# Optimization experiments

Measured on AMD Instinct MI355X. Metric: run time of the kernel, lower is better.

Reference implementation:

```python
import jax, jax.numpy as jnp
import numpy as np

V = 32000; DM = 512; DS = 64; K = 4; INNER = 2048; KK = 3
B = 4; N = 512; LOOPS = 6; H_CYCLES = 2; POWER = 2


def _ln(x, g, b, eps=1e-5):
    mu = jnp.mean(x, -1, keepdims=True)
    var = jnp.mean(jnp.square(x - mu), -1, keepdims=True)
    return (x - mu) * jax.lax.rsqrt(var + eps) * g + b


def _sn(W, u):
    # torch spectral_norm: one power iteration (no grad through u,v), sigma differentiable through W
    v = W.T @ u
    v = v / (jnp.linalg.norm(v) + 1e-12)
    u2 = W @ v
    u2 = u2 / (jnp.linalg.norm(u2) + 1e-12)
    u2 = jax.lax.stop_gradient(u2)
    v = jax.lax.stop_gradient(v)
    sigma = u2 @ (W @ v)
    return W / sigma


def _block(Q_in, p):
    Qn = _ln(Q_in, p['g1'], p['b1'])                       # [B,N,d]
    qp = Qn.mean(1)                                        # [B,d]
    Wq = _sn(p['hqW'], p['uq'])
    Wk = _sn(p['hkW'], p['uk'])
    Oq = (qp @ Wq.T).reshape(-1, DM, DS)                   # [B,d,D]
    Ok = (qp @ Wk.T).reshape(-1, DM, DS)
    Pq = jax.nn.elu(jnp.einsum('bnd,bde->bne', Qn, Oq) + p['BQ']) + 1.0
    Pk = jax.nn.elu(jnp.einsum('bnd,bde->bne', Qn, Ok) + p['BK']) + 1.0
    Wm = jnp.maximum(jnp.einsum('bne,bme->bnm', Pq, Pk), 0.0) ** POWER  # [B,N,N]
    Att = jnp.einsum('bnm,bmd->bnd', Wm, Qn)
    Nrm = jnp.abs(Wm.sum(-1)) + 1.0                        # [B,N]
    m = Att / Nrm[..., None] - Qn
    mp = m @ p['mW'].T + p['mb']
    Qi = Q_in + jax.nn.softplus(p['dt']) * mp
    Qn2 = _ln(Qi, p['g2'], p['b2'])
    GU = Qn2 @ p['WupW'].T                                 # [B,N,2*inner]
    G, U = GU[..., :INNER], GU[..., INNER:]
    H = jax.nn.silu(G) * U
    Ht = jnp.transpose(H, (0, 2, 1))                       # [B,inner,N]
    Hc = jax.lax.conv_general_dilated(Ht, p['convW'], (1,), [(1, 1)],
                                      dimension_numbers=('NCH', 'OIH', 'NCH'),
                                      feature_group_count=INNER)
    Hc = jnp.transpose(Hc, (0, 2, 1))
    return Qi + Hc @ p['WdownW'].T


def _run(Q, bp):
    for i in range(K):
        Q = _block(Q, {k: v[i] for k, v in bp.items()})
    return Q


def setup_inputs() -> dict:
    key = jax.random.key(0)
    ks = iter(jax.random.split(key, 48))
    nrm = lambda s, std=0.02: jax.random.normal(next(ks), s, jnp.float32) * std
    inp = {}
    inp['inputs'] = jax.random.randint(next(ks), (B, N), 0, V, jnp.int32)
    inp['labels'] = jax.random.randint(next(ks), (B, N), 0, V, jnp.int32)
    inp['halted'] = jnp.ones((B,), bool)
    inp['steps'] = jnp.zeros((B,), jnp.int32)
    inp['carry_hidden'] = jnp.zeros((B, N, DM), jnp.float32)
    inp['carry_inputs'] = jnp.zeros((B, N), jnp.int32)
    inp['carry_labels'] = jnp.zeros((B, N), jnp.int32)
    inp['embedding'] = nrm((V, DM))
    inp['pos_emb'] = nrm((8192, DM))
    inp['in_g'] = jnp.ones((DM,), jnp.float32)
    inp['in_b'] = jnp.zeros((DM,), jnp.float32)
    inp['init_hidden'] = nrm((DM,))
    inp['dt'] = jnp.full((K,), 0.1, jnp.float32)
    inp['mW'] = nrm((K, DM, DM))
    inp['mb'] = jnp.zeros((K, DM), jnp.float32)
    inp['hqW'] = nrm((K, DM * DS, DM))
    inp['hkW'] = nrm((K, DM * DS, DM))
    uq = jax.random.normal(next(ks), (K, DM * DS), jnp.float32)
    uk = jax.random.normal(next(ks), (K, DM * DS), jnp.float32)
    inp['uq'] = uq / jnp.linalg.norm(uq, axis=-1, keepdims=True)
    inp['uk'] = uk / jnp.linalg.norm(uk, axis=-1, keepdims=True)
    inp['BQ'] = nrm((K, DS))
    inp['BK'] = nrm((K, DS))
    inp['g1'] = jnp.ones((K, DM), jnp.float32)
    inp['b1'] = jnp.zeros((K, DM), jnp.float32)
    inp['g2'] = jnp.ones((K, DM), jnp.float32)
    inp['b2'] = jnp.zeros((K, DM), jnp.float32)
    inp['WupW'] = nrm((K, 2 * INNER, DM))
    inp['convW'] = nrm((K, INNER, 1, KK))
    inp['WdownW'] = nrm((K, DM, INNER))
    inp['fin_g'] = jnp.ones((DM,), jnp.float32)
    inp['fin_b'] = jnp.zeros((DM,), jnp.float32)
    inp['halt_W'] = nrm((1, DM))
    inp['halt_b'] = jnp.full((1,), -5.0, jnp.float32)
    inp['lm_head'] = nrm((V, DM))
    return inp


def reference(inputs, labels, halted, steps, carry_hidden, carry_inputs, carry_labels,
              embedding, pos_emb, in_g, in_b, init_hidden, dt, mW, mb, hqW, hkW, uq, uk,
              BQ, BK, g1, b1, g2, b2, WupW, convW, WdownW, fin_g, fin_b, halt_W, halt_b, lm_head):
    bp = dict(dt=dt, mW=mW, mb=mb, hqW=hqW, hkW=hkW, uq=uq, uk=uk, BQ=BQ, BK=BK,
              g1=g1, b1=b1, g2=g2, b2=b2, WupW=WupW, convW=convW, WdownW=WdownW)
    new_hidden = jnp.where(halted[:, None, None], init_hidden, carry_hidden)
    new_steps = jnp.where(halted, jnp.zeros_like(steps), steps)
    new_inputs = jnp.where(halted[:, None], inputs, carry_inputs)
    X = _ln(embedding[new_inputs] + pos_emb[:inputs.shape[1]][None], in_g, in_b)
    Q = new_hidden
    for _ in range(H_CYCLES - 1):  # no_grad burn-in
        Q = jax.lax.stop_gradient(_run(Q + X, bp))
    Q = _run(Q + X, bp)            # gradient pass (L_cycles = 1)
    Qf = _ln(Q, fin_g, fin_b)
    logits = Qf @ lm_head.T
    halt_logits = Qf.mean(1) @ halt_W.T + halt_b
    new_steps = new_steps + 1
    new_halted = new_steps >= LOOPS
    return logits, halt_logits, jax.lax.stop_gradient(Q), new_steps, new_halted
```

## Files before the change

kernel.cpp:

```cpp
#include <hip/hip_runtime.h>
#include <stdint.h>

#define DMD 512
#define NSEQ 512
#define NBATCH 4
#define WROWS 32768
#define VOCAB 32000

#define OFF_HALT   65536000L
#define OFF_Q      65536004L
#define OFF_STEPS  66584580L
#define OFF_HALTED 66584584L

typedef __attribute__((ext_vector_type(8))) short short8v;
typedef __attribute__((ext_vector_type(4))) float f32x4;

__device__ __forceinline__ ushort f2bf(float f){
  uint u = __builtin_bit_cast(uint, f);
  u += 0x7fffu + ((u >> 16) & 1u);
  return (ushort)(u >> 16);
}
__device__ __forceinline__ float bf2f(ushort h){
  return __builtin_bit_cast(float, (uint)h << 16);
}

__device__ __forceinline__ float block_reduce_sum256(float v, float* red){
  int t = threadIdx.x;
  red[t] = v; __syncthreads();
  for (int o = 128; o; o >>= 1){
    if (t < o) red[t] += red[t+o];
    __syncthreads();
  }
  float r = red[0]; __syncthreads();
  return r;
}

__global__ void k_ln(const float* __restrict__ in, float* __restrict__ outf,
                     ushort* __restrict__ outb,
                     const float* __restrict__ g, const float* __restrict__ b){
  __shared__ float red[256];
  long r = blockIdx.x; int t = threadIdx.x;
  const float* x = in + r*DMD;
  float v0 = x[t], v1 = x[t+256];
  float mu = block_reduce_sum256(v0+v1, red) * (1.f/DMD);
  float d0 = v0-mu, d1 = v1-mu;
  float var = block_reduce_sum256(d0*d0+d1*d1, red) * (1.f/DMD);
  float rs = rsqrtf(var + 1e-5f);
  float o0 = d0*rs*g[t] + b[t];
  float o1 = d1*rs*g[t+256] + b[t+256];
  if (outf){ outf[r*DMD+t] = o0; outf[r*DMD+t+256] = o1; }
  if (outb){ outb[r*DMD+t] = f2bf(o0); outb[r*DMD+t+256] = f2bf(o1); }
}

__global__ void k_ln_add(float* __restrict__ Qa, const float* __restrict__ X,
                         float* __restrict__ outf, ushort* __restrict__ outb,
                         const float* __restrict__ g, const float* __restrict__ b){
  __shared__ float red[256];
  long r = blockIdx.x; int t = threadIdx.x;
  float* x = Qa + r*DMD;
  const float* xx = X + r*DMD;
  float v0 = x[t]+xx[t], v1 = x[t+256]+xx[t+256];
  x[t] = v0; x[t+256] = v1;
  float mu = block_reduce_sum256(v0+v1, red) * (1.f/DMD);
  float d0 = v0-mu, d1 = v1-mu;
  float var = block_reduce_sum256(d0*d0+d1*d1, red) * (1.f/DMD);
  float rs = rsqrtf(var + 1e-5f);
  float o0 = d0*rs*g[t] + b[t];
  float o1 = d1*rs*g[t+256] + b[t+256];
  if (outf){ outf[r*DMD+t] = o0; outf[r*DMD+t+256] = o1; }
  if (outb){ outb[r*DMD+t] = f2bf(o0); outb[r*DMD+t+256] = f2bf(o1); }
}

__global__ void k_embed_ln(const int* __restrict__ inputs, const int* __restrict__ cinputs,
                           const int* __restrict__ halted32,
                           const float* __restrict__ emb, const float* __restrict__ pos,
                           const float* __restrict__ g, const float* __restrict__ b,
                           float* __restrict__ X){
  __shared__ float red[256];
  int r = blockIdx.x; int t = threadIdx.x;
  int n = r & 511;
  bool hall = (halted32[0] != 0);
  int tok = hall ? inputs[r] : cinputs[r];
  const float* e = emb + (long)tok*DMD;
  const float* p = pos + (long)n*DMD;
  float v0 = e[t]+p[t], v1 = e[t+256]+p[t+256];
  float mu = block_reduce_sum256(v0+v1, red) * (1.f/DMD);
  float d0 = v0-mu, d1 = v1-mu;
  float var = block_reduce_sum256(d0*d0+d1*d1, red) * (1.f/DMD);
  float rs = rsqrtf(var + 1e-5f);
  X[(long)r*DMD+t]     = d0*rs*g[t]     + b[t];
  X[(long)r*DMD+t+256] = d1*rs*g[t+256] + b[t+256];
}

__global__ void k_sn_v(const float* __restrict__ hqW, const float* __restrict__ hkW,
                       const float* __restrict__ uq, const float* __restrict__ uk,
                       float* __restrict__ vraw, ushort* __restrict__ Wbf){
  __shared__ float red[2048];
  int z = blockIdx.y; int k = z >> 1, qk = z & 1;
  const float* W = (qk ? hkW : hqW) + (long)k*WROWS*DMD;
  const float* u = (qk ? uk : uq) + (long)k*WROWS;
  ushort* Wb = Wbf ? (Wbf + (long)z*WROWS*DMD) : nullptr;
  int t = threadIdx.x;
  int c4 = (t & 127) * 4;
  int rsub = t >> 7;
  int r0 = blockIdx.x * 256;
  float4 acc = {0.f,0.f,0.f,0.f};
  if (Wb){
    for (int r = rsub; r < 256; r += 4){
      long off = (long)(r0+r)*DMD + c4;
      float4 w = *(const float4*)(W + off);
      float uu = u[r0+r];
      acc.x += w.x*uu; acc.y += w.y*uu; acc.z += w.z*uu; acc.w += w.w*uu;
      ushort4 o; o.x = f2bf(w.x); o.y = f2bf(w.y); o.z = f2bf(w.z); o.w = f2bf(w.w);
      *(ushort4*)(Wb + off) = o;
    }
  } else {
    for (int r = rsub; r < 256; r += 4){
      long off = (long)(r0+r)*DMD + c4;
      float4 w = *(const float4*)(W + off);
      float uu = u[r0+r];
      acc.x += w.x*uu; acc.y += w.y*uu; acc.z += w.z*uu; acc.w += w.w*uu;
    }
  }
  red[rsub*512 + c4+0] = acc.x; red[rsub*512 + c4+1] = acc.y;
  red[rsub*512 + c4+2] = acc.z; red[rsub*512 + c4+3] = acc.w;
  __syncthreads();
  if (rsub == 0){
    #pragma unroll
    for (int i = 0; i < 4; i++){
      int c = c4 + i;
      float s = red[c] + red[512+c] + red[1024+c] + red[1536+c];
      atomicAdd(&vraw[z*DMD + c], s);
    }
  }
}

__global__ void k_sn_norm(float* __restrict__ vraw){
  __shared__ float red[512];
  int z = blockIdx.x; int t = threadIdx.x;
  float* v = vraw + z*DMD;
  float x = v[t];
  red[t] = x*x; __syncthreads();
  for (int o = 256; o; o >>= 1){
    if (t < o) red[t] += red[t+o];
    __syncthreads();
  }
  float nrm = sqrtf(red[0]);
  v[t] = x / (nrm + 1e-12f);
}

__global__ void k_sn_s(const float* __restrict__ hqW, const float* __restrict__ hkW,
                       const float* __restrict__ vraw, float* __restrict__ ssq){
  int z = blockIdx.y; int k = z >> 1, qk = z & 1;
  const float* W = (qk ? hkW : hqW) + (long)k*WROWS*DMD;
  const float* v = vraw + z*DMD;
  int wave = threadIdx.x >> 6, lane = threadIdx.x & 63;
  float vreg[8];
  #pragma unroll
  for (int i = 0; i < 8; i++) vreg[i] = v[lane + 64*i];
  int r0 = blockIdx.x*256 + wave*64;
  float acc = 0.f;
  for (int r = r0; r < r0+64; r++){
    float p = 0.f;
    #pragma unroll
    for (int i = 0; i < 8; i++)
      p += W[(long)r*DMD + lane + 64*i] * vreg[i];
    for (int off = 32; off; off >>= 1) p += __shfl_down(p, off);
    if (lane == 0) acc += p*p;
  }
  if (lane == 0) atomicAdd(&ssq[z], acc);
}

__global__ void k_sn_s_bf(const ushort* __restrict__ Wbf, const float* __restrict__ vraw,
                          float* __restrict__ ssq){
  int z = blockIdx.y;
  const ushort* W = Wbf + (long)z*WROWS*DMD;
  const float* v = vraw + z*DMD;
  int wave = threadIdx.x >> 6, lane = threadIdx.x & 63;
  float vreg[8];
  #pragma unroll
  for (int i = 0; i < 8; i++) vreg[i] = v[lane*8 + i];
  int r0 = blockIdx.x*256 + wave*64;
  float acc = 0.f;
  for (int r = r0; r < r0+64; r++){
    short8v wv = *(const short8v*)&W[(long)r*DMD + lane*8];
    float p = 0.f;
    #pragma unroll
    for (int i = 0; i < 8; i++)
      p += bf2f((ushort)wv[i]) * vreg[i];
    for (int off = 32; off; off >>= 1) p += __shfl_down(p, off);
    if (lane == 0) acc += p*p;
  }
  if (lane == 0) atomicAdd(&ssq[z], acc);
}

__global__ void k_sn_fin(const float* __restrict__ ssq, float* __restrict__ sgm){
  int t = threadIdx.x;
  if (t < 8){
    float s2 = ssq[t];
    sgm[t] = s2 / (sqrtf(s2) + 1e-12f);
  }
}

__global__ void k_proj(const float* __restrict__ hqW, const float* __restrict__ hkW,
                       const float* __restrict__ qp, const float* __restrict__ sgm,
                       ushort* __restrict__ OqT, ushort* __restrict__ OkT, int k){
  int z = blockIdx.y;
  const float* W = (z ? hkW : hqW) + (long)k*WROWS*DMD;
  ushort* O = z ? OkT : OqT;
  float inv = 1.f / sgm[k*2 + z];
  int wave = threadIdx.x >> 6, lane = threadIdx.x & 63;
  long r = (long)blockIdx.x*4 + wave;
  float a0=0,a1=0,a2=0,a3=0;
  for (int j = lane; j < DMD; j += 64){
    float w = W[r*DMD + j];
    a0 += w*qp[j]; a1 += w*qp[DMD+j]; a2 += w*qp[2*DMD+j]; a3 += w*qp[3*DMD+j];
  }
  for (int off = 32; off; off >>= 1){
    a0 += __shfl_down(a0,off); a1 += __shfl_down(a1,off);
    a2 += __shfl_down(a2,off); a3 += __shfl_down(a3,off);
  }
  if (lane == 0){
    int d = (int)(r >> 6), e = (int)(r & 63);
    long o = (long)e*512 + d;
    O[o] = f2bf(a0*inv); O[32768+o] = f2bf(a1*inv);
    O[2*32768+o] = f2bf(a2*inv); O[3*32768+o] = f2bf(a3*inv);
  }
}

__global__ void k_proj_bf(const ushort* __restrict__ Wbf, const float* __restrict__ qp,
                          const float* __restrict__ sgm,
                          ushort* __restrict__ OqT, ushort* __restrict__ OkT, int k){
  int z = blockIdx.y;
  const ushort* W = Wbf + (long)(k*2 + z)*WROWS*DMD;
  ushort* O = z ? OkT : OqT;
  float inv = 1.f / sgm[k*2 + z];
  int wave = threadIdx.x >> 6, lane = threadIdx.x & 63;
  float qpr[4][8];
  #pragma unroll
  for (int b = 0; b < 4; b++)
    #pragma unroll
    for (int i = 0; i < 8; i++)
      qpr[b][i] = qp[b*512 + lane*8 + i];
  long r = (long)blockIdx.x*4 + wave;
  short8v wv = *(const short8v*)&W[r*DMD + lane*8];
  float w[8];
  #pragma unroll
  for (int i = 0; i < 8; i++) w[i] = bf2f((ushort)wv[i]);
  float a0=0,a1=0,a2=0,a3=0;
  #pragma unroll
  for (int i = 0; i < 8; i++){
    a0 += w[i]*qpr[0][i]; a1 += w[i]*qpr[1][i];
    a2 += w[i]*qpr[2][i]; a3 += w[i]*qpr[3][i];
  }
  for (int off = 32; off; off >>= 1){
    a0 += __shfl_down(a0,off); a1 += __shfl_down(a1,off);
    a2 += __shfl_down(a2,off); a3 += __shfl_down(a3,off);
  }
  if (lane == 0){
    int d = (int)(r >> 6), e = (int)(r & 63);
    long o = (long)e*512 + d;
    O[o] = f2bf(a0*inv); O[32768+o] = f2bf(a1*inv);
    O[2*32768+o] = f2bf(a2*inv); O[3*32768+o] = f2bf(a3*inv);
  }
}

template<int BM, int BN, int WM, int WN, int EPI, int BFOUT, int DUAL>
__global__ __launch_bounds__(256) void mm_bt(
    const ushort* __restrict__ A, const ushort* __restrict__ B, void* __restrict__ C,
    int N, int K, long sA, long sB, long sC,
    const float* __restrict__ bias, const float* __restrict__ bias2,
    const float* __restrict__ res, const float* __restrict__ dtp, int dtidx,
    float* __restrict__ aux)
{
  __shared__ ushort As[BM*64];
  __shared__ ushort Bs[BN*64];
  const int z = blockIdx.z;
  const float* biasz = bias;
  if (DUAL){
    A += (long)(z & 3)*sA;
    if (z >= 4) biasz = bias2;
  } else {
    A += (long)z*sA;
  }
  B += (long)z*sB;
  const int tm = blockIdx.y*BM, tn = DUAL ? 0 : blockIdx.x*BN;
  const int tid = threadIdx.x;
  const int wid = tid >> 6, lane = tid & 63;
// ... 37 lines not shown
      }
      #pragma unroll
      for (int j = 0; j < FN; j++){
        int row = wc*WN + j*16 + ln15;
        bfr[j] = *(const short8v*)&Bs[row*64 + (((ks*4+kq) ^ (row&7))*8)];
      }
      #pragma unroll
      for (int i = 0; i < FM; i++)
        #pragma unroll
        for (int j = 0; j < FN; j++)
          acc[i][j] = __builtin_amdgcn_mfma_f32_16x16x32_bf16(af[i], bfr[j], acc[i][j], 0, 0, 0);
    }
    __syncthreads();
  }

  float sp = 0.f;
  if (EPI == 3) sp = log1pf(expf(dtp[dtidx]));
  float* Cf = (float*)C + (long)z*sC;
  ushort* Cb = (ushort*)C + (long)z*sC;
  const float* rz = res ? (res + (long)z*sC) : nullptr;
  const float* nrmz = (EPI == 5) ? (bias + (long)z*512) : nullptr;
  #pragma unroll
  for (int i = 0; i < FM; i++){
    int row0 = tm + wr*WM + i*16 + kq*4;
    #pragma unroll
    for (int j = 0; j < FN; j++){
      int col = tn + wc*WN + j*16 + ln15;
      #pragma unroll
      for (int r = 0; r < 4; r++){
        int row = row0 + r;
        long idx = (long)row*N + col;
        float v = acc[i][j][r];
        if (EPI == 1){ v += biasz[col]; v = v > 0.f ? v : expm1f(v); v += 1.f; }
        else if (EPI == 2){ v = fmaxf(v, 0.f); v = v*v; }
        else if (EPI == 3){ v = rz[idx] + sp*(v + biasz[col]); }
        else if (EPI == 4){ v = v + rz[idx]; if (aux) aux[idx] = v; }
        else if (EPI == 5){ v = v / nrmz[row] - rz[idx]; }
        if (BFOUT) Cb[idx] = f2bf(v);
        else       Cf[idx] = v;
      }
    }
  }
}

__global__ void k_tr(const float* __restrict__ Qn, ushort* __restrict__ QnT){
  __shared__ float t[64][65];
  int b = blockIdx.z;
  int n0 = blockIdx.x*64, d0 = blockIdx.y*64;
  int tx = threadIdx.x & 63, ty = threadIdx.x >> 6;
  #pragma unroll
  for (int i = 0; i < 64; i += 4)
    t[ty+i][tx] = Qn[(long)b*262144 + (long)(n0+ty+i)*512 + d0+tx];
  __syncthreads();
  #pragma unroll
  for (int i = 0; i < 64; i += 4)
    QnT[(long)b*262144 + (long)(d0+ty+i)*512 + n0+tx] = f2bf(t[tx][ty+i]);
}

__global__ void k_qinit(const int* __restrict__ halted32, const float* __restrict__ ih,
                        const float* __restrict__ ch, float* __restrict__ Qa){
  long i = (long)blockIdx.x*512 + threadIdx.x;
  int c = (int)(i & 511);
  Qa[i] = (halted32[0] != 0) ? ih[c] : ch[i];
}

__global__ void k_qp1(const float* __restrict__ Qn, float* __restrict__ part){
  int b = blockIdx.x, c = blockIdx.y, t = threadIdx.x;
  const float* base = Qn + (long)b*262144 + (long)c*32*512;
  float acc = 0.f;
  #pragma unroll
  for (int n = 0; n < 32; n++) acc += base[n*512 + t];
  part[((long)b*16 + c)*512 + t] = acc;
}
__global__ void k_qp2(const float* __restrict__ part, float* __restrict__ qp){
  int b = blockIdx.x, t = threadIdx.x;
  float s = 0.f;
  #pragma unroll
  for (int c = 0; c < 16; c++) s += part[((long)b*16 + c)*512 + t];
  qp[b*512 + t] = s * (1.f/512.f);
}

__global__ void k_rowsum_bf(const ushort* __restrict__ Wm, float* __restrict__ Nrm){
  __shared__ float red[256];
  long r = blockIdx.x; int t = threadIdx.x;
  const ushort* x = Wm + r*NSEQ;
  float s = block_reduce_sum256(bf2f(x[t]) + bf2f(x[t+256]), red);
  if (t == 0) Nrm[r] = fabsf(s) + 1.f;
}

__global__ void k_convfuse(const ushort* __restrict__ GU, const float* __restrict__ w,
                           ushort* __restrict__ Hc){
  int r = blockIdx.x;
  int n = r & 511;
  int c = threadIdx.x * 8;
  long base = (long)r*4096 + c;
  float o[8] = {};
  {
    if (n > 0){
      short8v gv = *(const short8v*)&GU[base-4096];
      short8v uv = *(const short8v*)&GU[base-4096+2048];
      #pragma unroll
      for (int i = 0; i < 8; i++){
        float g = bf2f((ushort)gv[i]), u = bf2f((ushort)uv[i]);
        o[i] += g/(1.f+expf(-g))*u * w[(c+i)*3+0];
      }
    }
    {
      short8v gv = *(const short8v*)&GU[base];
      short8v uv = *(const short8v*)&GU[base+2048];
      #pragma unroll
      for (int i = 0; i < 8; i++){
        float g = bf2f((ushort)gv[i]), u = bf2f((ushort)uv[i]);
        o[i] += g/(1.f+expf(-g))*u * w[(c+i)*3+1];
      }
    }
    if (n < 511){
      short8v gv = *(const short8v*)&GU[base+4096];
      short8v uv = *(const short8v*)&GU[base+4096+2048];
      #pragma unroll
      for (int i = 0; i < 8; i++){
        float g = bf2f((ushort)gv[i]), u = bf2f((ushort)uv[i]);
        o[i] += g/(1.f+expf(-g))*u * w[(c+i)*3+2];
      }
    }
  }
  short8v ov;
  #pragma unroll
  for (int i = 0; i < 8; i++) ov[i] = (short)f2bf(o[i]);
  *(short8v*)&Hc[(long)r*2048 + c] = ov;
}

__global__ void k_cvt(const float* __restrict__ in, ushort* __restrict__ out){
  long i = ((long)blockIdx.x*256 + threadIdx.x)*4;
  float4 v = *(const float4*)(in + i);
  ushort4 o;
  o.x = f2bf(v.x); o.y = f2bf(v.y); o.z = f2bf(v.z); o.w = f2bf(v.w);
  *(ushort4*)(out + i) = o;
}

__global__ void k_halt1(const float* __restrict__ Qf, const float* __restrict__ hW,
                        float* __restrict__ hpart){
  __shared__ float red[256];
  int b = blockIdx.x, c = blockIdx.y, t = threadIdx.x;
  const float* base = Qf + (long)b*262144 + (long)c*32*512;
  float acc = 0.f;
  for (int i = t; i < 32*512; i += 256)
    acc += base[i] * hW[i & 511];
  float s = block_reduce_sum256(acc, red);
  if (t == 0) hpart[b*16 + c] = s;
}

__global__ void k_fin(const int* __restrict__ halted32, const int* __restrict__ steps,
                      const float* __restrict__ hpart, const float* __restrict__ hb,
                      float* __restrict__ o_halt, float* __restrict__ o_steps,
                      float* __restrict__ o_halted){
  int t = threadIdx.x;
  if (t < NBATCH){
    float s = 0.f;
    for (int c = 0; c < 16; c++) s += hpart[t*16 + c];
    o_halt[t] = s*(1.f/512.f) + hb[0];
    bool hall = (halted32[0] != 0);
    int ns = (hall ? 0 : steps[t]) + 1;
    o_steps[t] = (float)ns;
    o_halted[t] = ns >= 6 ? 1.f : 0.f;
  }
}

extern "C" void kernel_launch(void* const* d_in, const int* in_sizes, int n_in,
                              void* d_out, int out_size, void* d_ws, size_t ws_size,
                              hipStream_t stream)
{
  const int*     inputs       = (const int*)d_in[0];
  const int*     halted32     = (const int*)d_in[2];
  const int*     steps        = (const int*)d_in[3];
  const float*   carry_hidden = (const float*)d_in[4];
// ... 18 lines not shown
  const float*   b2   = (const float*)d_in[24];
  const float*   WupW = (const float*)d_in[25];
  const float*   convW= (const float*)d_in[26];
  const float*   WdownW=(const float*)d_in[27];
  const float*   fin_g= (const float*)d_in[28];
  const float*   fin_b= (const float*)d_in[29];
  const float*   halt_W=(const float*)d_in[30];
  const float*   halt_b=(const float*)d_in[31];
  const float*   lm_head=(const float*)d_in[32];
  float* out = (float*)d_out;

  float* ws = (float*)d_ws;
  float*  X    = ws;
  float*  Qa   = ws +  1048576;
  float*  Qb   = ws +  2097152;
  float*  Qn   = ws +  3145728;
  ushort* GU_bf  = (ushort*)(ws +  4194304);
  ushort* Hc_bf  = (ushort*)(ws +  8388608);
  ushort* m_bf   = (ushort*)(ws + 10485760);
  ushort* Wm_bf  = (ushort*)(ws + 11010048);
  ushort* QnT_bf = (ushort*)(ws + 11534336);
  ushort* Pq_bf  = (ushort*)(ws + 12058624);
  ushort* OqT    = (ushort*)(ws + 12189696);
  ushort* lm_bf  = (ushort*)(ws +  4194304);
  ushort* Qn_bf  = (ushort*)(ws + 13369344);
  ushort* mW_bf  = (ushort*)(ws + 13893632);
  ushort* Wup_bf = (ushort*)(ws + 14417920);
  ushort* Wdn_bf = (ushort*)(ws + 18612224);
  float*  qp   = ws + 20709376;
  float*  Nrm  = ws + 20711424;
  float*  vraw = ws + 20713472;
  float*  ssq  = ws + 20717568;
  float*  sgm  = ws + 20717632;
  float*  qp_part = ws + 20717696;
  float*  hpart   = ws + 20750464;
  ushort* W_bf = (ushort*)(ws + 20750528);
  const size_t NEED_BF = (size_t)(20750528 + 67108864) * 4;
  const bool useBf = ws_size >= NEED_BF;

  k_cvt<<<1024, 256, 0, stream>>>(mW, mW_bf);
  k_cvt<<<8192, 256, 0, stream>>>(WupW, Wup_bf);
  k_cvt<<<4096, 256, 0, stream>>>(WdownW, Wdn_bf);

  hipMemsetAsync(vraw, 0, (4096+64)*sizeof(float), stream);
  k_sn_v<<<dim3(128,8), 512, 0, stream>>>(hqW, hkW, uq, uk, vraw,
                                          useBf ? W_bf : nullptr);
  k_sn_norm<<<8, 512, 0, stream>>>(vraw);
  if (useBf)
    k_sn_s_bf<<<dim3(128,8), 256, 0, stream>>>(W_bf, vraw, ssq);
  else
    k_sn_s<<<dim3(128,8), 256, 0, stream>>>(hqW, hkW, vraw, ssq);
  k_sn_fin<<<1, 64, 0, stream>>>(ssq, sgm);

  k_embed_ln<<<2048, 256, 0, stream>>>(inputs, carry_inputs, halted32,
                                       embedding, pos_emb, in_g, in_b, X);
  k_qinit<<<2048, 512, 0, stream>>>(halted32, init_hidden, carry_hidden, Qa);

  for (int cyc = 0; cyc < 2; cyc++){
    for (int k = 0; k < 4; k++){
      if (k == 0)
        k_ln_add<<<2048, 256, 0, stream>>>(Qa, X, Qn, Qn_bf, g1 + k*DMD, b1 + k*DMD);
      else
        k_ln<<<2048, 256, 0, stream>>>(Qa, Qn, Qn_bf, g1 + k*DMD, b1 + k*DMD);
      k_tr<<<dim3(8,8,4), 256, 0, stream>>>(Qn, QnT_bf);
      k_qp1<<<dim3(4,16), 512, 0, stream>>>(Qn, qp_part);
      k_qp2<<<4, 512, 0, stream>>>(qp_part, qp);
      if (useBf)
        k_proj_bf<<<dim3(8192,2), 256, 0, stream>>>(W_bf, qp, sgm, OqT, OqT + 131072, k);
      else
        k_proj<<<dim3(8192,2), 256, 0, stream>>>(hqW, hkW, qp, sgm, OqT, OqT + 131072, k);
      mm_bt<64,64,32,32,1,1,1><<<dim3(1,8,8), 256, 0, stream>>>(
          Qn_bf, OqT, Pq_bf, 64, 512, 262144, 32768, 32768,
          BQb + k*64, BKb + k*64, nullptr, nullptr, 0, nullptr);
      mm_bt<64,64,32,32,2,1,0><<<dim3(8,8,4), 256, 0, stream>>>(
          Pq_bf, Pq_bf + 131072, Wm_bf, 512, 64, 32768, 32768, 262144,
          nullptr, nullptr, nullptr, nullptr, 0, nullptr);
      k_rowsum_bf<<<2048, 256, 0, stream>>>(Wm_bf, Nrm);
      mm_bt<64,64,32,32,5,1,0><<<dim3(8,8,4), 256, 0, stream>>>(
          Wm_bf, QnT_bf, m_bf, 512, 512, 262144, 262144, 262144,
          Nrm, nullptr, Qn, nullptr, 0, nullptr);
      mm_bt<64,64,32,32,3,0,0><<<dim3(8,32,1), 256, 0, stream>>>(
          m_bf, mW_bf + (long)k*262144, Qb, 512, 512, 0, 0, 0,
          mb + k*DMD, nullptr, Qa, dt, k, nullptr);
      k_ln<<<2048, 256, 0, stream>>>(Qb, nullptr, Qn_bf, g2 + k*DMD, b2 + k*DMD);
      mm_bt<128,128,64,64,0,1,0><<<dim3(32,16,1), 256, 0, stream>>>(
          Qn_bf, Wup_bf + (long)k*2097152, GU_bf, 4096, 512, 0, 0, 0,
          nullptr, nullptr, nullptr, nullptr, 0, nullptr);
      k_convfuse<<<2048, 256, 0, stream>>>(GU_bf, convW + (long)k*2048*3, Hc_bf);
      float* aux = (cyc == 1 && k == 3) ? (out + OFF_Q) : nullptr;
      mm_bt<64,64,32,32,4,0,0><<<dim3(8,32,1), 256, 0, stream>>>(
          Hc_bf, Wdn_bf + (long)k*1048576, Qa, 512, 2048, 0, 0, 0,
          nullptr, nullptr, Qb, nullptr, 0, aux);
    }
  }

  k_ln<<<2048, 256, 0, stream>>>(Qa, Qn, Qn_bf, fin_g, fin_b);
  k_cvt<<<16000, 256, 0, stream>>>(lm_head, lm_bf);
  mm_bt<128,128,64,64,0,0,0><<<dim3(250,16,1), 256, 0, stream>>>(
      Qn_bf, lm_bf, out, 32000, 512, 0, 0, 0,
      nullptr, nullptr, nullptr, nullptr, 0, nullptr);
  k_halt1<<<dim3(4,16), 256, 0, stream>>>(Qn, halt_W, hpart);
  k_fin<<<1, 64, 0, stream>>>(halted32, steps, hpart, halt_b,
                              out + OFF_HALT, out + OFF_STEPS, out + OFF_HALTED);
}
```

Measured before the change: 1.730 ms.

## Fuse layernorm with transpose, pooling, halt head; fold spectral norm and rowsum into GEMMs

Replaces the per-row layernorm kernels with a multi-row warp-level kernel that also writes the transposed bf16 copy, partial sequence means, the residual add and initial-state selection, and the halt dot product. This removes the separate transpose, qp1, qinit and halt kernels along with the fp32 Qn buffer. The spectral-norm sigma is now computed inside the first-cycle projection kernel and applied in the Pq/Pk GEMM epilogue, and the Wm row sums are accumulated with atomics in the Wm GEMM epilogue instead of a separate rowsum kernel. The costs are more atomics, a 64-entry sum repeated in every epilogue thread, and residuals read from bf16 Qn instead of fp32, which slightly lowers precision.

```diff
diff --git a/kernel.cpp b/kernel.cpp
--- a/kernel.cpp
+++ b/kernel.cpp
@@ -35,40 +35,99 @@
   return r;
 }
 
-__global__ void k_ln(const float* __restrict__ in, float* __restrict__ outf,
-                     ushort* __restrict__ outb,
-                     const float* __restrict__ g, const float* __restrict__ b){
-  __shared__ float red[256];
-  long r = blockIdx.x; int t = threadIdx.x;
-  const float* x = in + r*DMD;
-  float v0 = x[t], v1 = x[t+256];
-  float mu = block_reduce_sum256(v0+v1, red) * (1.f/DMD);
-  float d0 = v0-mu, d1 = v1-mu;
-  float var = block_reduce_sum256(d0*d0+d1*d1, red) * (1.f/DMD);
-  float rs = rsqrtf(var + 1e-5f);
-  float o0 = d0*rs*g[t] + b[t];
-  float o1 = d1*rs*g[t+256] + b[t+256];
-  if (outf){ outf[r*DMD+t] = o0; outf[r*DMD+t+256] = o1; }
-  if (outb){ outb[r*DMD+t] = f2bf(o0); outb[r*DMD+t+256] = f2bf(o1); }
-}
-
-__global__ void k_ln_add(float* __restrict__ Qa, const float* __restrict__ X,
-                         float* __restrict__ outf, ushort* __restrict__ outb,
-                         const float* __restrict__ g, const float* __restrict__ b){
-  __shared__ float red[256];
-  long r = blockIdx.x; int t = threadIdx.x;
-  float* x = Qa + r*DMD;
-  const float* xx = X + r*DMD;
-  float v0 = x[t]+xx[t], v1 = x[t+256]+xx[t+256];
-  x[t] = v0; x[t+256] = v1;
-  float mu = block_reduce_sum256(v0+v1, red) * (1.f/DMD);
-  float d0 = v0-mu, d1 = v1-mu;
-  float var = block_reduce_sum256(d0*d0+d1*d1, red) * (1.f/DMD);
-  float rs = rsqrtf(var + 1e-5f);
-  float o0 = d0*rs*g[t] + b[t];
-  float o1 = d1*rs*g[t+256] + b[t+256];
-  if (outf){ outf[r*DMD+t] = o0; outf[r*DMD+t+256] = o1; }
-  if (outb){ outb[r*DMD+t] = f2bf(o0); outb[r*DMD+t+256] = f2bf(o1); }
+template<int MODE, int TR, int QP, int HALT>
+__global__ __launch_bounds__(512) void k_ln1(
+    const float* in, float* QaW, const float* X,
+    const int* halted32, const float* ih, const float* ch,
+    ushort* __restrict__ outb, ushort* __restrict__ outT,
+    float* __restrict__ qp_part,
+    const float* __restrict__ g, const float* __restrict__ b,
+    const float* __restrict__ hW, float* __restrict__ hpart)
+{
+  __shared__ ushort lt[TR ? 32 : 1][TR ? 514 : 1];
+  __shared__ float red[QP ? 4096 : 1];
+  const int bb = blockIdx.y, rg = blockIdx.x;
+  const int n0 = rg*32;
+  const int tid = threadIdx.x, wave = tid >> 6, lane = tid & 63;
+  const int c8 = lane*8;
+  float qacc[8] = {};
+  #pragma unroll
+  for (int rr = 0; rr < 4; rr++){
+    const int n = n0 + wave*4 + rr;
+    const long rowo = (long)bb*262144 + (long)n*512;
+    float x[8];
+    if (MODE == 1){
+      bool hall = (halted32[0] != 0);
+      #pragma unroll
+      for (int i = 0; i < 8; i++){
+        float base = hall ? ih[c8+i] : ch[rowo + c8 + i];
+        x[i] = base + X[rowo + c8 + i];
+      }
+      #pragma unroll
+      for (int i = 0; i < 8; i++) QaW[rowo + c8 + i] = x[i];
+    } else if (MODE == 2){
+      #pragma unroll
+      for (int i = 0; i < 8; i++) x[i] = in[rowo + c8 + i] + X[rowo + c8 + i];
+      #pragma unroll
+      for (int i = 0; i < 8; i++) QaW[rowo + c8 + i] = x[i];
+    } else {
+      float4 a0 = *(const float4*)(in + rowo + c8);
+      float4 a1 = *(const float4*)(in + rowo + c8 + 4);
+      x[0]=a0.x; x[1]=a0.y; x[2]=a0.z; x[3]=a0.w;
+      x[4]=a1.x; x[5]=a1.y; x[6]=a1.z; x[7]=a1.w;
+    }
+    float s = 0.f, sq = 0.f;
+    #pragma unroll
+    for (int i = 0; i < 8; i++){ s += x[i]; sq += x[i]*x[i]; }
+    #pragma unroll
+    for (int m = 32; m; m >>= 1){
+      s  += __shfl_xor(s, m);
+      sq += __shfl_xor(sq, m);
+    }
+    float mu = s*(1.f/512.f);
+    float var = sq*(1.f/512.f) - mu*mu;
+    float rs = rsqrtf(var + 1e-5f);
+    float hd = 0.f;
+    short8v ov;
+    #pragma unroll
+    for (int i = 0; i < 8; i++){
+      float o = (x[i]-mu)*rs*g[c8+i] + b[c8+i];
+      ov[i] = (short)f2bf(o);
+      if (QP) qacc[i] += o;
+      if (HALT) hd += o * hW[c8+i];
+    }
+    *(short8v*)&outb[rowo + c8] = ov;
+    if (TR) *(short8v*)&lt[n & 31][c8] = ov;
+    if (HALT){
+      #pragma unroll
+      for (int m = 32; m; m >>= 1) hd += __shfl_xor(hd, m);
+      if (lane == 0) atomicAdd(&hpart[bb], hd);
+    }
+  }
+  if (QP){
+    #pragma unroll
+    for (int i = 0; i < 8; i++) red[wave*512 + c8 + i] = qacc[i];
+    __syncthreads();
+    if (wave == 0){
+      #pragma unroll
+      for (int i = 0; i < 8; i++){
+        int c = c8 + i;
+        float s = 0.f;
+        #pragma unroll
+        for (int w = 0; w < 8; w++) s += red[w*512 + c];
+        qp_part[((long)bb*16 + rg)*512 + c] = s;
+      }
+    }
+  }
+  if (TR){
+    __syncthreads();
+    #pragma unroll 4
+    for (int p = 0; p < 32; p++){
+      int d = p*16 + (tid >> 5);
+      int n = tid & 31;
+      outT[(long)bb*262144 + (long)d*512 + n0 + n] = lt[n][d];
+    }
+  }
 }
 
 __global__ void k_embed_ln(const int* __restrict__ inputs, const int* __restrict__ cinputs,
@@ -92,44 +151,45 @@
   X[(long)r*DMD+t+256] = d1*rs*g[t+256] + b[t+256];
 }
 
-__global__ void k_sn_v(const float* __restrict__ hqW, const float* __restrict__ hkW,
-                       const float* __restrict__ uq, const float* __restrict__ uk,
-                       float* __restrict__ vraw, ushort* __restrict__ Wbf){
-  __shared__ float red[2048];
+__global__ __launch_bounds__(512) void k_sn_v(
+    const float* __restrict__ hqW, const float* __restrict__ hkW,
+    const float* __restrict__ uq, const float* __restrict__ uk,
+    float* __restrict__ vraw, ushort* __restrict__ Wbf){
+  __shared__ float red[4096];
   int z = blockIdx.y; int k = z >> 1, qk = z & 1;
   const float* W = (qk ? hkW : hqW) + (long)k*WROWS*DMD;
   const float* u = (qk ? uk : uq) + (long)k*WROWS;
   ushort* Wb = Wbf ? (Wbf + (long)z*WROWS*DMD) : nullptr;
   int t = threadIdx.x;
-  int c4 = (t & 127) * 4;
-  int rsub = t >> 7;
+  int c8 = (t & 63) * 8;
+  int rsub = t >> 6;
   int r0 = blockIdx.x * 256;
-  float4 acc = {0.f,0.f,0.f,0.f};
-  if (Wb){
-    for (int r = rsub; r < 256; r += 4){
-      long off = (long)(r0+r)*DMD + c4;
-      float4 w = *(const float4*)(W + off);
-      float uu = u[r0+r];
-      acc.x += w.x*uu; acc.y += w.y*uu; acc.z += w.z*uu; acc.w += w.w*uu;
-      ushort4 o; o.x = f2bf(w.x); o.y = f2bf(w.y); o.z = f2bf(w.z); o.w = f2bf(w.w);
-      *(ushort4*)(Wb + off) = o;
-    }
-  } else {
-    for (int r = rsub; r < 256; r += 4){
-      long off = (long)(r0+r)*DMD + c4;
-      float4 w = *(const float4*)(W + off);
-      float uu = u[r0+r];
-      acc.x += w.x*uu; acc.y += w.y*uu; acc.z += w.z*uu; acc.w += w.w*uu;
-    }
-  }
-  red[rsub*512 + c4+0] = acc.x; red[rsub*512 + c4+1] = acc.y;
-  red[rsub*512 + c4+2] = acc.z; red[rsub*512 + c4+3] = acc.w;
+  float acc[8] = {};
+  for (int r = rsub; r < 256; r += 8){
+    long off = (long)(r0+r)*DMD + c8;
+    float4 w0 = *(const float4*)(W + off);
+    float4 w1 = *(const float4*)(W + off + 4);
+    float uu = u[r0+r];
+    float wv[8] = {w0.x,w0.y,w0.z,w0.w,w1.x,w1.y,w1.z,w1.w};
+    #pragma unroll
+    for (int i = 0; i < 8; i++) acc[i] += wv[i]*uu;
+    if (Wb){
+      short8v o;
+      #pragma unroll
+      for (int i = 0; i < 8; i++) o[i] = (short)f2bf(wv[i]);
+      *(short8v*)(Wb + off) = o;
+    }
+  }
+  #pragma unroll
+  for (int i = 0; i < 8; i++) red[rsub*512 + c8 + i] = acc[i];
   __syncthreads();
   if (rsub == 0){
     #pragma unroll
-    for (int i = 0; i < 4; i++){
-      int c = c4 + i;
-      float s = red[c] + red[512+c] + red[1024+c] + red[1536+c];
+    for (int i = 0; i < 8; i++){
+      int c = c8 + i;
+      float s = 0.f;
+      #pragma unroll
+      for (int w = 0; w < 8; w++) s += red[w*512 + c];
       atomicAdd(&vraw[z*DMD + c], s);
     }
   }
@@ -150,7 +210,7 @@
 }
 
 __global__ void k_sn_s(const float* __restrict__ hqW, const float* __restrict__ hkW,
-                       const float* __restrict__ vraw, float* __restrict__ ssq){
+                       const float* __restrict__ vraw, float* __restrict__ ssqp){
   int z = blockIdx.y; int k = z >> 1, qk = z & 1;
   const float* W = (qk ? hkW : hqW) + (long)k*WROWS*DMD;
   const float* v = vraw + z*DMD;
@@ -168,47 +228,63 @@
     for (int off = 32; off; off >>= 1) p += __shfl_down(p, off);
     if (lane == 0) acc += p*p;
   }
-  if (lane == 0) atomicAdd(&ssq[z], acc);
-}
-
-__global__ void k_sn_s_bf(const ushort* __restrict__ Wbf, const float* __restrict__ vraw,
-                          float* __restrict__ ssq){
+  if (lane == 0) atomicAdd(&ssqp[z*64 + (blockIdx.x & 63)], acc);
+}
+
+__global__ void k_proj_bf(const ushort* __restrict__ Wbf, const float* __restrict__ qp,
+                          const float* __restrict__ vraw, float* __restrict__ ssqp,
+                          ushort* __restrict__ OqT, ushort* __restrict__ OkT,
+                          int k, int doSn){
   int z = blockIdx.y;
-  const ushort* W = Wbf + (long)z*WROWS*DMD;
-  const float* v = vraw + z*DMD;
+  const ushort* W = Wbf + (long)(k*2 + z)*WROWS*DMD;
+  ushort* O = z ? OkT : OqT;
   int wave = threadIdx.x >> 6, lane = threadIdx.x & 63;
+  float qpr[4][8];
+  #pragma unroll
+  for (int b = 0; b < 4; b++)
+    #pragma unroll
+    for (int i = 0; i < 8; i++)
+      qpr[b][i] = qp[b*512 + lane*8 + i];
   float vreg[8];
-  #pragma unroll
-  for (int i = 0; i < 8; i++) vreg[i] = v[lane*8 + i];
-  int r0 = blockIdx.x*256 + wave*64;
-  float acc = 0.f;
-  for (int r = r0; r < r0+64; r++){
-    short8v wv = *(const short8v*)&W[(long)r*DMD + lane*8];
-    float p = 0.f;
-    #pragma unroll
-    for (int i = 0; i < 8; i++)
-      p += bf2f((ushort)wv[i]) * vreg[i];
-    for (int off = 32; off; off >>= 1) p += __shfl_down(p, off);
-    if (lane == 0) acc += p*p;
-  }
-  if (lane == 0) atomicAdd(&ssq[z], acc);
-}
-
-__global__ void k_sn_fin(const float* __restrict__ ssq, float* __restrict__ sgm){
-  int t = threadIdx.x;
-  if (t < 8){
-    float s2 = ssq[t];
-    sgm[t] = s2 / (sqrtf(s2) + 1e-12f);
+  if (doSn){
+    #pragma unroll
+    for (int i = 0; i < 8; i++) vreg[i] = vraw[(k*2 + z)*512 + lane*8 + i];
+  }
+  long r = (long)blockIdx.x*4 + wave;
+  short8v wv = *(const short8v*)&W[r*DMD + lane*8];
+  float w[8];
+  #pragma unroll
+  for (int i = 0; i < 8; i++) w[i] = bf2f((ushort)wv[i]);
+  float a0=0,a1=0,a2=0,a3=0,a4=0;
+  #pragma unroll
+  for (int i = 0; i < 8; i++){
+    a0 += w[i]*qpr[0][i]; a1 += w[i]*qpr[1][i];
+    a2 += w[i]*qpr[2][i]; a3 += w[i]*qpr[3][i];
+  }
+  if (doSn){
+    #pragma unroll
+    for (int i = 0; i < 8; i++) a4 += w[i]*vreg[i];
+  }
+  for (int off = 32; off; off >>= 1){
+    a0 += __shfl_down(a0,off); a1 += __shfl_down(a1,off);
+    a2 += __shfl_down(a2,off); a3 += __shfl_down(a3,off);
+    a4 += __shfl_down(a4,off);
+  }
+  if (lane == 0){
+    int d = (int)(r >> 6), e = (int)(r & 63);
+    long o = (long)e*512 + d;
+    O[o] = f2bf(a0); O[32768+o] = f2bf(a1);
+    O[2*32768+o] = f2bf(a2); O[3*32768+o] = f2bf(a3);
+    if (doSn) atomicAdd(&ssqp[(k*2 + z)*64 + ((int)blockIdx.x & 63)], a4*a4);
   }
 }
 
 __global__ void k_proj(const float* __restrict__ hqW, const float* __restrict__ hkW,
-                       const float* __restrict__ qp, const float* __restrict__ sgm,
+                       const float* __restrict__ qp,
                        ushort* __restrict__ OqT, ushort* __restrict__ OkT, int k){
   int z = blockIdx.y;
   const float* W = (z ? hkW : hqW) + (long)k*WROWS*DMD;
   ushort* O = z ? OkT : OqT;
-  float inv = 1.f / sgm[k*2 + z];
   int wave = threadIdx.x >> 6, lane = threadIdx.x & 63;
   long r = (long)blockIdx.x*4 + wave;
   float a0=0,a1=0,a2=0,a3=0;
@@ -223,55 +299,19 @@
   if (lane == 0){
     int d = (int)(r >> 6), e = (int)(r & 63);
     long o = (long)e*512 + d;
-    O[o] = f2bf(a0*inv); O[32768+o] = f2bf(a1*inv);
-    O[2*32768+o] = f2bf(a2*inv); O[3*32768+o] = f2bf(a3*inv);
-  }
-}
-
-__global__ void k_proj_bf(const ushort* __restrict__ Wbf, const float* __restrict__ qp,
-                          const float* __restrict__ sgm,
-                          ushort* __restrict__ OqT, ushort* __restrict__ OkT, int k){
-  int z = blockIdx.y;
-  const ushort* W = Wbf + (long)(k*2 + z)*WROWS*DMD;
-  ushort* O = z ? OkT : OqT;
-  float inv = 1.f / sgm[k*2 + z];
-  int wave = threadIdx.x >> 6, lane = threadIdx.x & 63;
-  float qpr[4][8];
-  #pragma unroll
-  for (int b = 0; b < 4; b++)
-    #pragma unroll
-    for (int i = 0; i < 8; i++)
-      qpr[b][i] = qp[b*512 + lane*8 + i];
-  long r = (long)blockIdx.x*4 + wave;
-  short8v wv = *(const short8v*)&W[r*DMD + lane*8];
-  float w[8];
-  #pragma unroll
-  for (int i = 0; i < 8; i++) w[i] = bf2f((ushort)wv[i]);
-  float a0=0,a1=0,a2=0,a3=0;
-  #pragma unroll
-  for (int i = 0; i < 8; i++){
-    a0 += w[i]*qpr[0][i]; a1 += w[i]*qpr[1][i];
-    a2 += w[i]*qpr[2][i]; a3 += w[i]*qpr[3][i];
-  }
-  for (int off = 32; off; off >>= 1){
-    a0 += __shfl_down(a0,off); a1 += __shfl_down(a1,off);
-    a2 += __shfl_down(a2,off); a3 += __shfl_down(a3,off);
-  }
-  if (lane == 0){
-    int d = (int)(r >> 6), e = (int)(r & 63);
-    long o = (long)e*512 + d;
-    O[o] = f2bf(a0*inv); O[32768+o] = f2bf(a1*inv);
-    O[2*32768+o] = f2bf(a2*inv); O[3*32768+o] = f2bf(a3*inv);
-  }
-}
-
-template<int BM, int BN, int WM, int WN, int EPI, int BFOUT, int DUAL>
+    O[o] = f2bf(a0); O[32768+o] = f2bf(a1);
+    O[2*32768+o] = f2bf(a2); O[3*32768+o] = f2bf(a3);
+  }
+}
+
+template<int BM, int BN, int WM, int WN, int EPI, int BFOUT, int DUAL, int RSUM>
 __global__ __launch_bounds__(256) void mm_bt(
     const ushort* __restrict__ A, const ushort* __restrict__ B, void* __restrict__ C,
     int N, int K, long sA, long sB, long sC,
     const float* __restrict__ bias, const float* __restrict__ bias2,
-    const float* __restrict__ res, const float* __restrict__ dtp, int dtidx,
-    float* __restrict__ aux)
+    const float* __restrict__ res, const ushort* __restrict__ resb,
+    const float* __restrict__ dtp, int dtidx,
+    float* __restrict__ aux, const float* __restrict__ ssqp)
 {
   __shared__ ushort As[BM*64];
   __shared__ ushort Bs[BN*64];
@@ -339,12 +379,20 @@
     __syncthreads();
   }
 
-  float sp = 0.f;
+  float sp = 0.f, invs = 1.f;
   if (EPI == 3) sp = log1pf(expf(dtp[dtidx]));
+  if (EPI == 1){
+    const float* sq = ssqp + (DUAL ? (z >> 2)*64 : 0);
+    float s2 = 0.f;
+    for (int i = 0; i < 64; i++) s2 += sq[i];
+    invs = (sqrtf(s2) + 1e-12f) / s2;
+  }
   float* Cf = (float*)C + (long)z*sC;
   ushort* Cb = (ushort*)C + (long)z*sC;
   const float* rz = res ? (res + (long)z*sC) : nullptr;
+  const ushort* rzb = resb ? (resb + (long)z*sC) : nullptr;
   const float* nrmz = (EPI == 5) ? (bias + (long)z*512) : nullptr;
+  float rsv[FM][4] = {};
   #pragma unroll
   for (int i = 0; i < FM; i++){
     int row0 = tm + wr*WM + i*16 + kq*4;
@@ -356,61 +404,39 @@
         int row = row0 + r;
         long idx = (long)row*N + col;
         float v = acc[i][j][r];
-        if (EPI == 1){ v += biasz[col]; v = v > 0.f ? v : expm1f(v); v += 1.f; }
-        else if (EPI == 2){ v = fmaxf(v, 0.f); v = v*v; }
+        if (EPI == 1){ v = v*invs + biasz[col]; v = v > 0.f ? v : expm1f(v); v += 1.f; }
+        else if (EPI == 2){ v = fmaxf(v, 0.f); v = v*v; if (RSUM) rsv[i][r] += v; }
         else if (EPI == 3){ v = rz[idx] + sp*(v + biasz[col]); }
         else if (EPI == 4){ v = v + rz[idx]; if (aux) aux[idx] = v; }
-        else if (EPI == 5){ v = v / nrmz[row] - rz[idx]; }
+        else if (EPI == 5){ v = v/(fabsf(nrmz[row])+1.f) - bf2f(rzb[idx]); }
         if (BFOUT) Cb[idx] = f2bf(v);
         else       Cf[idx] = v;
       }
     }
   }
-}
-
-__global__ void k_tr(const float* __restrict__ Qn, ushort* __restrict__ QnT){
-  __shared__ float t[64][65];
-  int b = blockIdx.z;
-  int n0 = blockIdx.x*64, d0 = blockIdx.y*64;
-  int tx = threadIdx.x & 63, ty = threadIdx.x >> 6;
-  #pragma unroll
-  for (int i = 0; i < 64; i += 4)
-    t[ty+i][tx] = Qn[(long)b*262144 + (long)(n0+ty+i)*512 + d0+tx];
-  __syncthreads();
-  #pragma unroll
-  for (int i = 0; i < 64; i += 4)
-    QnT[(long)b*262144 + (long)(d0+ty+i)*512 + n0+tx] = f2bf(t[tx][ty+i]);
-}
-
-__global__ void k_qinit(const int* __restrict__ halted32, const float* __restrict__ ih,
-                        const float* __restrict__ ch, float* __restrict__ Qa){
-  long i = (long)blockIdx.x*512 + threadIdx.x;
-  int c = (int)(i & 511);
-  Qa[i] = (halted32[0] != 0) ? ih[c] : ch[i];
-}
-
-__global__ void k_qp1(const float* __restrict__ Qn, float* __restrict__ part){
-  int b = blockIdx.x, c = blockIdx.y, t = threadIdx.x;
-  const float* base = Qn + (long)b*262144 + (long)c*32*512;
-  float acc = 0.f;
-  #pragma unroll
-  for (int n = 0; n < 32; n++) acc += base[n*512 + t];
-  part[((long)b*16 + c)*512 + t] = acc;
-}
-__global__ void k_qp2(const float* __restrict__ part, float* __restrict__ qp){
+  if (RSUM){
+    #pragma unroll
+    for (int i = 0; i < FM; i++){
+      #pragma unroll
+      for (int r = 0; r < 4; r++){
+        float x = rsv[i][r];
+        x += __shfl_xor(x, 1); x += __shfl_xor(x, 2);
+        x += __shfl_xor(x, 4); x += __shfl_xor(x, 8);
+        if (ln15 == 0)
+          atomicAdd(&aux[(long)z*512 + tm + wr*WM + i*16 + kq*4 + r], x);
+      }
+    }
+  }
+}
+
+__global__ void k_qp2(const float* __restrict__ part, float* __restrict__ qp,
+                      float* __restrict__ nrm_raw){
   int b = blockIdx.x, t = threadIdx.x;
   float s = 0.f;
   #pragma unroll
   for (int c = 0; c < 16; c++) s += part[((long)b*16 + c)*512 + t];
   qp[b*512 + t] = s * (1.f/512.f);
-}
-
-__global__ void k_rowsum_bf(const ushort* __restrict__ Wm, float* __restrict__ Nrm){
-  __shared__ float red[256];
-  long r = blockIdx.x; int t = threadIdx.x;
-  const ushort* x = Wm + r*NSEQ;
-  float s = block_reduce_sum256(bf2f(x[t]) + bf2f(x[t+256]), red);
-  if (t == 0) Nrm[r] = fabsf(s) + 1.f;
+  nrm_raw[b*512 + t] = 0.f;
 }
 
 __global__ void k_convfuse(const ushort* __restrict__ GU, const float* __restrict__ w,
@@ -420,33 +446,31 @@
   int c = threadIdx.x * 8;
   long base = (long)r*4096 + c;
   float o[8] = {};
+  if (n > 0){
+    short8v gv = *(const short8v*)&GU[base-4096];
+    short8v uv = *(const short8v*)&GU[base-4096+2048];
+    #pragma unroll
+    for (int i = 0; i < 8; i++){
+      float g = bf2f((ushort)gv[i]), u = bf2f((ushort)uv[i]);
+      o[i] += g/(1.f+expf(-g))*u * w[(c+i)*3+0];
+    }
+  }
   {
-    if (n > 0){
-      short8v gv = *(const short8v*)&GU[base-4096];
-      short8v uv = *(const short8v*)&GU[base-4096+2048];
-      #pragma unroll
-      for (int i = 0; i < 8; i++){
-        float g = bf2f((ushort)gv[i]), u = bf2f((ushort)uv[i]);
-        o[i] += g/(1.f+expf(-g))*u * w[(c+i)*3+0];
-      }
-    }
-    {
-      short8v gv = *(const short8v*)&GU[base];
-      short8v uv = *(const short8v*)&GU[base+2048];
-      #pragma unroll
-      for (int i = 0; i < 8; i++){
-        float g = bf2f((ushort)gv[i]), u = bf2f((ushort)uv[i]);
-        o[i] += g/(1.f+expf(-g))*u * w[(c+i)*3+1];
-      }
-    }
-    if (n < 511){
-      short8v gv = *(const short8v*)&GU[base+4096];
-      short8v uv = *(const short8v*)&GU[base+4096+2048];
-      #pragma unroll
-      for (int i = 0; i < 8; i++){
-        float g = bf2f((ushort)gv[i]), u = bf2f((ushort)uv[i]);
-        o[i] += g/(1.f+expf(-g))*u * w[(c+i)*3+2];
-      }
+    short8v gv = *(const short8v*)&GU[base];
+    short8v uv = *(const short8v*)&GU[base+2048];
+    #pragma unroll
+    for (int i = 0; i < 8; i++){
+      float g = bf2f((ushort)gv[i]), u = bf2f((ushort)uv[i]);
+      o[i] += g/(1.f+expf(-g))*u * w[(c+i)*3+1];
+    }
+  }
+  if (n < 511){
+    short8v gv = *(const short8v*)&GU[base+4096];
+    short8v uv = *(const short8v*)&GU[base+4096+2048];
+    #pragma unroll
+    for (int i = 0; i < 8; i++){
+      float g = bf2f((ushort)gv[i]), u = bf2f((ushort)uv[i]);
+      o[i] += g/(1.f+expf(-g))*u * w[(c+i)*3+2];
     }
   }
   short8v ov;
@@ -463,27 +487,13 @@
   *(ushort4*)(out + i) = o;
 }
 
-__global__ void k_halt1(const float* __restrict__ Qf, const float* __restrict__ hW,
-                        float* __restrict__ hpart){
-  __shared__ float red[256];
-  int b = blockIdx.x, c = blockIdx.y, t = threadIdx.x;
-  const float* base = Qf + (long)b*262144 + (long)c*32*512;
-  float acc = 0.f;
-  for (int i = t; i < 32*512; i += 256)
-    acc += base[i] * hW[i & 511];
-  float s = block_reduce_sum256(acc, red);
-  if (t == 0) hpart[b*16 + c] = s;
-}
-
 __global__ void k_fin(const int* __restrict__ halted32, const int* __restrict__ steps,
                       const float* __restrict__ hpart, const float* __restrict__ hb,
                       float* __restrict__ o_halt, float* __restrict__ o_steps,
                       float* __restrict__ o_halted){
   int t = threadIdx.x;
   if (t < NBATCH){
-    float s = 0.f;
-    for (int c = 0; c < 16; c++) s += hpart[t*16 + c];
-    o_halt[t] = s*(1.f/512.f) + hb[0];
+    o_halt[t] = hpart[t]*(1.f/512.f) + hb[0];
     bool hall = (halted32[0] != 0);
     int ns = (hall ? 0 : steps[t]) + 1;
     o_steps[t] = (float)ns;
@@ -532,7 +542,6 @@
   float*  X    = ws;
   float*  Qa   = ws +  1048576;
   float*  Qb   = ws +  2097152;
-  float*  Qn   = ws +  3145728;
   ushort* GU_bf  = (ushort*)(ws +  4194304);
   ushort* Hc_bf  = (ushort*)(ws +  8388608);
   ushort* m_bf   = (ushort*)(ws + 10485760);
@@ -545,79 +554,86 @@
   ushort* mW_bf  = (ushort*)(ws + 13893632);
   ushort* Wup_bf = (ushort*)(ws + 14417920);
   ushort* Wdn_bf = (ushort*)(ws + 18612224);
-  float*  qp   = ws + 20709376;
-  float*  Nrm  = ws + 20711424;
-  float*  vraw = ws + 20713472;
-  float*  ssq  = ws + 20717568;
-  float*  sgm  = ws + 20717632;
-  float*  qp_part = ws + 20717696;
-  float*  hpart   = ws + 20750464;
-  ushort* W_bf = (ushort*)(ws + 20750528);
-  const size_t NEED_BF = (size_t)(20750528 + 67108864) * 4;
+  float*  qp       = ws + 20709376;
+  float*  Nrm_raw  = ws + 20711424;
+  float*  vraw     = ws + 20713472;
+  float*  ssq_part = ws + 20717568;
+  float*  hpart    = ws + 20718080;
+  float*  qp_part  = ws + 20718144;
+  ushort* W_bf = (ushort*)(ws + 20750976);
+  const size_t NEED_BF = (size_t)(20750976 + 67108864) * 4;
   const bool useBf = ws_size >= NEED_BF;
 
   k_cvt<<<1024, 256, 0, stream>>>(mW, mW_bf);
   k_cvt<<<8192, 256, 0, stream>>>(WupW, Wup_bf);
   k_cvt<<<4096, 256, 0, stream>>>(WdownW, Wdn_bf);
 
-  hipMemsetAsync(vraw, 0, (4096+64)*sizeof(float), stream);
+  hipMemsetAsync(vraw, 0, 4672*sizeof(float), stream);
   k_sn_v<<<dim3(128,8), 512, 0, stream>>>(hqW, hkW, uq, uk, vraw,
                                           useBf ? W_bf : nullptr);
   k_sn_norm<<<8, 512, 0, stream>>>(vraw);
-  if (useBf)
-    k_sn_s_bf<<<dim3(128,8), 256, 0, stream>>>(W_bf, vraw, ssq);
-  else
-    k_sn_s<<<dim3(128,8), 256, 0, stream>>>(hqW, hkW, vraw, ssq);
-  k_sn_fin<<<1, 64, 0, stream>>>(ssq, sgm);
+  if (!useBf)
+    k_sn_s<<<dim3(128,8), 256, 0, stream>>>(hqW, hkW, vraw, ssq_part);
 
   k_embed_ln<<<2048, 256, 0, stream>>>(inputs, carry_inputs, halted32,
                                        embedding, pos_emb, in_g, in_b, X);
-  k_qinit<<<2048, 512, 0, stream>>>(halted32, init_hidden, carry_hidden, Qa);
 
   for (int cyc = 0; cyc < 2; cyc++){
     for (int k = 0; k < 4; k++){
-      if (k == 0)
-        k_ln_add<<<2048, 256, 0, stream>>>(Qa, X, Qn, Qn_bf, g1 + k*DMD, b1 + k*DMD);
+      if (k == 0){
+        if (cyc == 0)
+          k_ln1<1,1,1,0><<<dim3(16,4), 512, 0, stream>>>(
+              Qa, Qa, X, halted32, init_hidden, carry_hidden,
+              Qn_bf, QnT_bf, qp_part, g1 + k*DMD, b1 + k*DMD, nullptr, nullptr);
+        else
+          k_ln1<2,1,1,0><<<dim3(16,4), 512, 0, stream>>>(
+              Qa, Qa, X, nullptr, nullptr, nullptr,
+              Qn_bf, QnT_bf, qp_part, g1 + k*DMD, b1 + k*DMD, nullptr, nullptr);
+      } else {
+        k_ln1<0,1,1,0><<<dim3(16,4), 512, 0, stream>>>(
+            Qa, nullptr, nullptr, nullptr, nullptr, nullptr,
+            Qn_bf, QnT_bf, qp_part, g1 + k*DMD, b1 + k*DMD, nullptr, nullptr);
+      }
+      k_qp2<<<4, 512, 0, stream>>>(qp_part, qp, Nrm_raw);
+      if (useBf)
+        k_proj_bf<<<dim3(8192,2), 256, 0, stream>>>(
+            W_bf, qp, vraw, ssq_part, OqT, OqT + 131072, k, cyc == 0 ? 1 : 0);
       else
-        k_ln<<<2048, 256, 0, stream>>>(Qa, Qn, Qn_bf, g1 + k*DMD, b1 + k*DMD);
-      k_tr<<<dim3(8,8,4), 256, 0, stream>>>(Qn, QnT_bf);
-      k_qp1<<<dim3(4,16), 512, 0, stream>>>(Qn, qp_part);
-      k_qp2<<<4, 512, 0, stream>>>(qp_part, qp);
-      if (useBf)
-        k_proj_bf<<<dim3(8192,2), 256, 0, stream>>>(W_bf, qp, sgm, OqT, OqT + 131072, k);
-      else
-        k_proj<<<dim3(8192,2), 256, 0, stream>>>(hqW, hkW, qp, sgm, OqT, OqT + 131072, k);
-      mm_bt<64,64,32,32,1,1,1><<<dim3(1,8,8), 256, 0, stream>>>(
+        k_proj<<<dim3(8192,2), 256, 0, stream>>>(hqW, hkW, qp, OqT, OqT + 131072, k);
+      mm_bt<64,64,32,32,1,1,1,0><<<dim3(1,8,8), 256, 0, stream>>>(
           Qn_bf, OqT, Pq_bf, 64, 512, 262144, 32768, 32768,
-          BQb + k*64, BKb + k*64, nullptr, nullptr, 0, nullptr);
-      mm_bt<64,64,32,32,2,1,0><<<dim3(8,8,4), 256, 0, stream>>>(
+          BQb + k*64, BKb + k*64, nullptr, nullptr, nullptr, 0,
+          nullptr, ssq_part + k*128);
+      mm_bt<64,64,32,32,2,1,0,1><<<dim3(8,8,4), 256, 0, stream>>>(
           Pq_bf, Pq_bf + 131072, Wm_bf, 512, 64, 32768, 32768, 262144,
-          nullptr, nullptr, nullptr, nullptr, 0, nullptr);
-      k_rowsum_bf<<<2048, 256, 0, stream>>>(Wm_bf, Nrm);
-      mm_bt<64,64,32,32,5,1,0><<<dim3(8,8,4), 256, 0, stream>>>(
+          nullptr, nullptr, nullptr, nullptr, nullptr, 0, Nrm_raw, nullptr);
+      mm_bt<64,64,32,32,5,1,0,0><<<dim3(8,8,4), 256, 0, stream>>>(
           Wm_bf, QnT_bf, m_bf, 512, 512, 262144, 262144, 262144,
-          Nrm, nullptr, Qn, nullptr, 0, nullptr);
-      mm_bt<64,64,32,32,3,0,0><<<dim3(8,32,1), 256, 0, stream>>>(
+          Nrm_raw, nullptr, nullptr, Qn_bf, nullptr, 0, nullptr, nullptr);
+      mm_bt<64,64,32,32,3,0,0,0><<<dim3(8,32,1), 256, 0, stream>>>(
           m_bf, mW_bf + (long)k*262144, Qb, 512, 512, 0, 0, 0,
-          mb + k*DMD, nullptr, Qa, dt, k, nullptr);
-      k_ln<<<2048, 256, 0, stream>>>(Qb, nullptr, Qn_bf, g2 + k*DMD, b2 + k*DMD);
-      mm_bt<128,128,64,64,0,1,0><<<dim3(32,16,1), 256, 0, stream>>>(
+          mb + k*DMD, nullptr, Qa, nullptr, dt, k, nullptr, nullptr);
+      k_ln1<0,0,0,0><<<dim3(16,4), 512, 0, stream>>>(
+          Qb, nullptr, nullptr, nullptr, nullptr, nullptr,
+          Qn_bf, nullptr, nullptr, g2 + k*DMD, b2 + k*DMD, nullptr, nullptr);
+      mm_bt<128,128,64,64,0,1,0,0><<<dim3(32,16,1), 256, 0, stream>>>(
           Qn_bf, Wup_bf + (long)k*2097152, GU_bf, 4096, 512, 0, 0, 0,
-          nullptr, nullptr, nullptr, nullptr, 0, nullptr);
+          nullptr, nullptr, nullptr, nullptr, nullptr, 0, nullptr, nullptr);
       k_convfuse<<<2048, 256, 0, stream>>>(GU_bf, convW + (long)k*2048*3, Hc_bf);
       float* aux = (cyc == 1 && k == 3) ? (out + OFF_Q) : nullptr;
-      mm_bt<64,64,32,32,4,0,0><<<dim3(8,32,1), 256, 0, stream>>>(
+      mm_bt<64,64,32,32,4,0,0,0><<<dim3(8,32,1), 256, 0, stream>>>(
           Hc_bf, Wdn_bf + (long)k*1048576, Qa, 512, 2048, 0, 0, 0,
-          nullptr, nullptr, Qb, nullptr, 0, aux);
-    }
-  }
-
-  k_ln<<<2048, 256, 0, stream>>>(Qa, Qn, Qn_bf, fin_g, fin_b);
+          nullptr, nullptr, Qb, nullptr, nullptr, 0, aux, nullptr);
+    }
+  }
+
+  k_ln1<0,0,0,1><<<dim3(16,4), 512, 0, stream>>>(
+      Qa, nullptr, nullptr, nullptr, nullptr, nullptr,
+      Qn_bf, nullptr, nullptr, fin_g, fin_b, halt_W, hpart);
   k_cvt<<<16000, 256, 0, stream>>>(lm_head, lm_bf);
-  mm_bt<128,128,64,64,0,0,0><<<dim3(250,16,1), 256, 0, stream>>>(
+  mm_bt<128,128,64,64,0,0,0,0><<<dim3(250,16,1), 256, 0, stream>>>(
       Qn_bf, lm_bf, out, 32000, 512, 0, 0, 0,
-      nullptr, nullptr, nullptr, nullptr, 0, nullptr);
-  k_halt1<<<dim3(4,16), 256, 0, stream>>>(Qn, halt_W, hpart);
+      nullptr, nullptr, nullptr, nullptr, nullptr, 0, nullptr, nullptr);
   k_fin<<<1, 64, 0, stream>>>(halted32, steps, hpart, halt_b,
                               out + OFF_HALT, out + OFF_STEPS, out + OFF_HALTED);
 }
```

Measured after the change: 2.635 ms. 1.52x slower.
